# Performance work log

Hardware: AMD Instinct MI355X
Metric: run time of the kernel (lower is better)

## Reference

```python
import jax, jax.numpy as jnp
import numpy as np

B, L, D, K_LIN, T = 32, 512, 1024, 7, 8  # T = 1 identity ('root') + 7 linear experts


def setup_inputs() -> dict:
    key = jax.random.key(0)
    k0, k1, k2 = jax.random.split(key, 3)
    actions = jax.random.normal(k0, (B, L, D), dtype=jnp.float32)
    action_type = jax.random.randint(k1, (B, L), 0, T)
    W = jax.random.normal(k2, (K_LIN, D, D), dtype=jnp.float32) * 0.02  # (K, out, in)
    b = jnp.zeros((K_LIN, D), dtype=jnp.float32)
    return {"actions": actions, "action_type": action_type, "W": W, "b": b}


def reference(actions, action_type, W, b):
    # Project padded actions through ALL experts (matches original ModuleDict loop).
    # proj: (B, L, K_LIN, D) ; W is (K, out, in) so contract over input dim i.
    proj = jnp.einsum('bli,koi->blko', actions, W) + b[None, None, :, :]
    # 'root' expert is nn.Identity -> stacked first (dict insertion order).
    p = jnp.concatenate([actions[:, :, None, :], proj], axis=2)  # (B, L, T, D)
    # One-hot mask built via scatter in the original == one_hot here.
    mask = jax.nn.one_hot(action_type, T, dtype=p.dtype)[..., None]  # (B, L, T, 1)
    embedded = (mask * p).sum(axis=2)  # (B, L, D)
    return embedded
```

## Files before the change

### kernel.cpp

```cpp
#include <hip/hip_runtime.h>


#define NTOK 16384
#define DDIM 1024
#define NEXP 7
#define BM 256
#define BN 256
#define BK 64
#define NKT (DDIM / BK)

#define WI_OFFS   16
#define WI_NTILES 32
#define WI_TABLE  64
#define WI_CTOK   512
#define WS_ABF_B  1048576
#define WS_WBF_B  (WS_ABF_B + NTOK * DDIM * 2)

typedef __attribute__((ext_vector_type(8))) short short8;
typedef __attribute__((ext_vector_type(4))) float f32x4;

__device__ __forceinline__ unsigned short f2bf(float f) {
    unsigned u = __float_as_uint(f);
    u += 0x7fff + ((u >> 16) & 1);
    return (unsigned short)(u >> 16);
}

__device__ __forceinline__ void gload16(const void* g, void* l) {
    __builtin_amdgcn_global_load_lds(
        (const __attribute__((address_space(1))) void*)g,
        (__attribute__((address_space(3))) void*)l, 16, 0, 0);
}

__global__ __launch_bounds__(1024) void routeconv_k(
    const int* __restrict__ type, int* __restrict__ wsi,
    const float* __restrict__ W, unsigned short* __restrict__ Wbf) {
    const int bid = blockIdx.x, tid = threadIdx.x;
    if (bid == 0) {
        __shared__ int h[16][8];
        __shared__ int base2[16][8];
        const int wave = tid >> 6, lane = tid & 63;
        const unsigned long long lt = (1ULL << lane) - 1;

        const int4* tsrc = (const int4*)(type + tid * 16);
        int4 v0 = tsrc[0], v1 = tsrc[1], v2 = tsrc[2], v3 = tsrc[3];
        int kv[16] = { v0.x, v0.y, v0.z, v0.w, v1.x, v1.y, v1.z, v1.w,
                       v2.x, v2.y, v2.z, v2.w, v3.x, v3.y, v3.z, v3.w };

        int cnt[8];
#pragma unroll
        for (int e = 0; e < 8; ++e) cnt[e] = 0;
#pragma unroll
        for (int i = 0; i < 16; ++i) {
#pragma unroll
            for (int e = 0; e < 8; ++e)
                cnt[e] += __popcll(__ballot(kv[i] == e));
        }
        if (lane == 0) {
#pragma unroll
            for (int e = 0; e < 8; ++e) h[wave][e] = cnt[e];
        }
        __syncthreads();

        if (tid == 0) {
            int acc = 0, t = 0;
            for (int e = 0; e < NEXP; ++e) {
                wsi[WI_OFFS + e] = acc;
                int run = acc;
                for (int w = 0; w < 16; ++w) { base2[w][e + 1] = run; run += h[w][e + 1]; }
                int nt = (run - acc + BM - 1) >> 8;
                for (int i = 0; i < nt; ++i) {
                    wsi[WI_TABLE + 2 * t] = e;
                    wsi[WI_TABLE + 2 * t + 1] = acc + i * BM;
                    ++t;
                }
                acc = run;
            }
            wsi[WI_OFFS + NEXP] = acc;
            wsi[WI_NTILES] = t;
            int run = acc;
            for (int w = 0; w < 16; ++w) { base2[w][0] = run; run += h[w][0]; }
        }
        __syncthreads();

        int rb[8];
#pragma unroll
        for (int e = 0; e < 8; ++e) rb[e] = base2[wave][e];
#pragma unroll
        for (int i = 0; i < 16; ++i) {
            int k = kv[i];
            int pos = 0;
#pragma unroll
            for (int e = 0; e < 8; ++e) {
                unsigned long long m = __ballot(k == e);
                int p = rb[e] + __popcll(m & lt);
                pos = (k == e) ? p : pos;
                rb[e] += __popcll(m);
            }
            wsi[WI_CTOK + pos] = tid * 16 + i;
        }
    } else {
        size_t i = ((size_t)(bid - 1) * 1024 + tid) * 16;
        const float4* src = (const float4*)(W + i);
        float4 v0 = src[0], v1 = src[1], v2 = src[2], v3 = src[3];
        short8 h0, h1;
        h0[0]=f2bf(v0.x); h0[1]=f2bf(v0.y); h0[2]=f2bf(v0.z); h0[3]=f2bf(v0.w);
        h0[4]=f2bf(v1.x); h0[5]=f2bf(v1.y); h0[6]=f2bf(v1.z); h0[7]=f2bf(v1.w);
        h1[0]=f2bf(v2.x); h1[1]=f2bf(v2.y); h1[2]=f2bf(v2.z); h1[3]=f2bf(v2.w);
        h1[4]=f2bf(v3.x); h1[5]=f2bf(v3.y); h1[6]=f2bf(v3.z); h1[7]=f2bf(v3.w);
        *(short8*)(Wbf + i) = h0;
        *(short8*)(Wbf + i + 8) = h1;
    }
}

__global__ __launch_bounds__(256) void aconv_k(
    const float* __restrict__ A, const int* __restrict__ wsi,
    unsigned short* __restrict__ Abf, float* __restrict__ out) {
    const int wave = threadIdx.x >> 6, lane = threadIdx.x & 63;
    const int s = blockIdx.x * 4 + wave;
    const int nlin = wsi[WI_OFFS + NEXP];
    const int tok = wsi[WI_CTOK + s];
    const float4* src = (const float4*)(A + (size_t)tok * DDIM);
    if (s >= nlin) {
        float4* d = (float4*)(out + (size_t)tok * DDIM);
#pragma unroll
        for (int j = 0; j < 4; ++j) d[lane + j * 64] = src[lane + j * 64];
    } else {
        float4 v0 = src[lane * 4 + 0], v1 = src[lane * 4 + 1];
        float4 v2 = src[lane * 4 + 2], v3 = src[lane * 4 + 3];
        short8 h0, h1;
        h0[0]=f2bf(v0.x); h0[1]=f2bf(v0.y); h0[2]=f2bf(v0.z); h0[3]=f2bf(v0.w);
        h0[4]=f2bf(v1.x); h0[5]=f2bf(v1.y); h0[6]=f2bf(v1.z); h0[7]=f2bf(v1.w);
        h1[0]=f2bf(v2.x); h1[1]=f2bf(v2.y); h1[2]=f2bf(v2.z); h1[3]=f2bf(v2.w);
        h1[4]=f2bf(v3.x); h1[5]=f2bf(v3.y); h1[6]=f2bf(v3.z); h1[7]=f2bf(v3.w);
        unsigned short* d = Abf + (size_t)s * DDIM + lane * 16;
        *(short8*)d = h0;
        *(short8*)(d + 8) = h1;
    }
}

#define TILE(Abase, Bbase, sNA, sNB, KT)                           \
    do {                                                           \
        short8 a1[8], b1[4];                                       \
        _Pragma("unroll")                                          \
        for (int m = 0; m < 8; ++m)                                \
            a1[m] = *(const short8*)(Abase + sl0 + m * 2048);      \
        _Pragma("unroll")                                          \
        for (int n = 0; n < 4; ++n)                                \
            b1[n] = *(const short8*)(Bbase + sl0 + n * 2048);      \
        if ((KT) + 1 < NKT) {                                      \
            const int ke_ = ((KT) + 1) * BK;                       \
            _Pragma("unroll")                                      \
            for (int q = 0; q < 4; ++q)                            \
                gload16(aSrc[q] + ke_, sNA + q * 8192);            \
            _Pragma("unroll")                                      \
            for (int q = 0; q < 4; ++q)                            \
                gload16(bSrc[q] + ke_, sNB + q * 8192);            \
        }                                                          \
        __builtin_amdgcn_s_setprio(1);                             \
        _Pragma("unroll")                                          \
        for (int m = 0; m < 8; ++m)                                \
            _Pragma("unroll")                                      \
            for (int n = 0; n < 4; ++n)                            \
                acc[m][n] = __builtin_amdgcn_mfma_f32_16x16x32_bf16(\
                    a1[m], b1[n], acc[m][n], 0, 0, 0);             \
        __builtin_amdgcn_s_setprio(0);                             \
        short8 a2[8], b2[4];                                       \
        _Pragma("unroll")                                          \
        for (int m = 0; m < 8; ++m)                                \
            a2[m] = *(const short8*)(Abase + sl1 + m * 2048);      \
        _Pragma("unroll")                                          \
        for (int n = 0; n < 4; ++n)                                \
            b2[n] = *(const short8*)(Bbase + sl1 + n * 2048);      \
        __builtin_amdgcn_s_setprio(1);                             \
        _Pragma("unroll")                                          \
        for (int m = 0; m < 8; ++m)                                \
            _Pragma("unroll")                                      \
            for (int n = 0; n < 4; ++n)                            \
                acc[m][n] = __builtin_amdgcn_mfma_f32_16x16x32_bf16(\
                    a2[m], b2[n], acc[m][n], 0, 0, 0);             \
        __builtin_amdgcn_s_setprio(0);                             \
        asm volatile("s_waitcnt vmcnt(0)" ::: "memory");           \
        __builtin_amdgcn_s_barrier();                              \
    } while (0)

__global__ __launch_bounds__(512, 2) void gemm_k(
    const unsigned short* __restrict__ Abf,
    const unsigned short* __restrict__ Wbf,
    const float* __restrict__ bias, float* __restrict__ out,
    const int* __restrict__ wsi) {
    const int bid = blockIdx.x;
    const int c = bid & 7;
    const int g = bid >> 3;
    const int ntiles = wsi[WI_NTILES];
    const int* offs = wsi + WI_OFFS;
    const int* tab  = wsi + WI_TABLE;
    const int* ctok = wsi + WI_CTOK;

    __shared__ unsigned short As0[BM * BK];
    __shared__ unsigned short As1[BM * BK];
    __shared__ unsigned short Bs0[BM * BK];
    __shared__ unsigned short Bs1[BM * BK];

    const int tid = threadIdx.x, lane = tid & 63, wave = tid >> 6;
    const int wr = wave >> 2, wc = wave & 3;
    const int lane15 = lane & 15;
    const int srow = lane >> 3;
    const int schunk = ((lane & 7) ^ srow) * 8;

    const int sl0 = (((lane >> 4)) ^ (lane & 7)) * 16;
    const int sl1 = ((4 | (lane >> 4)) ^ (lane & 7)) * 16;
    const char* aR0 = (const char*)As0 + wr * 16384 + lane15 * 128;
    const char* aR1 = (const char*)As1 + wr * 16384 + lane15 * 128;
    const char* bR0 = (const char*)Bs0 + wc * 8192 + lane15 * 128;
    const char* bR1 = (const char*)Bs1 + wc * 8192 + lane15 * 128;
    char* sA0 = (char*)As0 + wave * 1024;
    char* sA1 = (char*)As1 + wave * 1024;
    char* sB0 = (char*)Bs0 + wave * 1024;
    char* sB1 = (char*)Bs1 + wave * 1024;

    for (int rep = 0; rep < 2; ++rep) {
        const int q4 = g + 32 * rep;
        const int ty = (q4 >> 2) * 8 + c;
        const int tx = q4 & 3;
        if (ty >= ntiles) break;

        const int e     = tab[2 * ty];
        const int crow0 = tab[2 * ty + 1];
        const int nend  = offs[e + 1];
        const int col0  = tx * BN;
        const unsigned short* Wb = Wbf + (size_t)e * DDIM * DDIM;

        const unsigned short* aSrc[4];
        const unsigned short* bSrc[4];
#pragma unroll
        for (int q = 0; q < 4; ++q) {
            int r = min(crow0 + q * 64 + wave * 8 + srow, NTOK - 1);
            aSrc[q] = Abf + (size_t)r * DDIM + schunk;
            bSrc[q] = Wb + (size_t)(col0 + q * 64 + wave * 8 + srow) * DDIM + schunk;
        }

        f32x4 acc[8][4];
#pragma unroll
        for (int m = 0; m < 8; ++m)
#pragma unroll
            for (int n = 0; n < 4; ++n) acc[m][n] = (f32x4){0.f, 0.f, 0.f, 0.f};

#pragma unroll
        for (int q = 0; q < 4; ++q) gload16(aSrc[q], sA0 + q * 8192);
#pragma unroll
        for (int q = 0; q < 4; ++q) gload16(bSrc[q], sB0 + q * 8192);
        asm volatile("s_waitcnt vmcnt(0)" ::: "memory");
        __builtin_amdgcn_s_barrier();

        for (int kt2 = 0; kt2 < NKT / 2; ++kt2) {
            TILE(aR0, bR0, sA1, sB1, 2 * kt2);
            TILE(aR1, bR1, sA0, sB0, 2 * kt2 + 1);
        }

        const int crow4 = (lane >> 4) * 4;
        float bv[4];
#pragma unroll
        for (int n = 0; n < 4; ++n)
            bv[n] = bias[e * DDIM + col0 + wc * 64 + n * 16 + lane15];

#pragma unroll
        for (int m = 0; m < 8; ++m) {
#pragma unroll
            for (int r = 0; r < 4; ++r) {
                int gr = crow0 + wr * 128 + m * 16 + crow4 + r;
                if (gr >= nend) continue;
                int tok = ctok[gr];
                float* orow = out + (size_t)tok * DDIM + col0 + wc * 64 + lane15;
#pragma unroll
                for (int n = 0; n < 4; ++n)
                    orow[n * 16] = acc[m][n][r] + bv[n];
            }
        }
        __builtin_amdgcn_s_barrier();
    }
}

extern "C" void kernel_launch(void* const* d_in, const int* in_sizes, int n_in,
                              void* d_out, int out_size, void* d_ws, size_t ws_size,
                              hipStream_t stream) {
    const float* actions = (const float*)d_in[0];
    const int*   atype   = (const int*)d_in[1];
    const float* W       = (const float*)d_in[2];
    const float* bias    = (const float*)d_in[3];
    float* out = (float*)d_out;

    int* wsi = (int*)d_ws;
    unsigned short* Abf = (unsigned short*)((char*)d_ws + WS_ABF_B);
    unsigned short* Wbf = (unsigned short*)((char*)d_ws + WS_WBF_B);

    routeconv_k<<<1 + 448, 1024, 0, stream>>>(atype, wsi, W, Wbf);
    aconv_k<<<NTOK / 4, 256, 0, stream>>>(actions, wsi, Abf, out);
    gemm_k<<<256, 512, 0, stream>>>(Abf, Wbf, bias, out, wsi);
}
```

Baseline: 82.42 us.

## Fuse activation conversion into routing kernel and gather rows in GEMM

```diff
diff --git a/kernel.cpp b/kernel.cpp
--- a/kernel.cpp
+++ b/kernel.cpp
@@ -31,9 +31,11 @@
         (__attribute__((address_space(3))) void*)l, 16, 0, 0);
 }
 
-__global__ __launch_bounds__(1024) void routeconv_k(
+__global__ __launch_bounds__(1024) void prep_k(
     const int* __restrict__ type, int* __restrict__ wsi,
-    const float* __restrict__ W, unsigned short* __restrict__ Wbf) {
+    const float* __restrict__ W, unsigned short* __restrict__ Wbf,
+    const float* __restrict__ A, unsigned short* __restrict__ Abf,
+    float* __restrict__ out) {
     const int bid = blockIdx.x, tid = threadIdx.x;
     if (bid == 0) {
         __shared__ int h[16][8];
@@ -52,7 +54,7 @@
 #pragma unroll
         for (int i = 0; i < 16; ++i) {
 #pragma unroll
-            for (int e = 0; e < 8; ++e)
+            for (int e = 1; e < 8; ++e)
                 cnt[e] += __popcll(__ballot(kv[i] == e));
         }
         if (lane == 0) {
@@ -77,28 +79,26 @@
             }
             wsi[WI_OFFS + NEXP] = acc;
             wsi[WI_NTILES] = t;
-            int run = acc;
-            for (int w = 0; w < 16; ++w) { base2[w][0] = run; run += h[w][0]; }
         }
         __syncthreads();
 
         int rb[8];
 #pragma unroll
-        for (int e = 0; e < 8; ++e) rb[e] = base2[wave][e];
+        for (int e = 1; e < 8; ++e) rb[e] = base2[wave][e];
 #pragma unroll
         for (int i = 0; i < 16; ++i) {
             int k = kv[i];
-            int pos = 0;
-#pragma unroll
-            for (int e = 0; e < 8; ++e) {
+            int pos = -1;
+#pragma unroll
+            for (int e = 1; e < 8; ++e) {
                 unsigned long long m = __ballot(k == e);
                 int p = rb[e] + __popcll(m & lt);
                 pos = (k == e) ? p : pos;
                 rb[e] += __popcll(m);
             }
-            wsi[WI_CTOK + pos] = tid * 16 + i;
-        }
-    } else {
+            if (k > 0) wsi[WI_CTOK + pos] = tid * 16 + i;
+        }
+    } else if (bid <= 448) {
         size_t i = ((size_t)(bid - 1) * 1024 + tid) * 16;
         const float4* src = (const float4*)(W + i);
         float4 v0 = src[0], v1 = src[1], v2 = src[2], v3 = src[3];
@@ -109,32 +109,26 @@
         h1[4]=f2bf(v3.x); h1[5]=f2bf(v3.y); h1[6]=f2bf(v3.z); h1[7]=f2bf(v3.w);
         *(short8*)(Wbf + i) = h0;
         *(short8*)(Wbf + i + 8) = h1;
-    }
-}
-
-__global__ __launch_bounds__(256) void aconv_k(
-    const float* __restrict__ A, const int* __restrict__ wsi,
-    unsigned short* __restrict__ Abf, float* __restrict__ out) {
-    const int wave = threadIdx.x >> 6, lane = threadIdx.x & 63;
-    const int s = blockIdx.x * 4 + wave;
-    const int nlin = wsi[WI_OFFS + NEXP];
-    const int tok = wsi[WI_CTOK + s];
-    const float4* src = (const float4*)(A + (size_t)tok * DDIM);
-    if (s >= nlin) {
-        float4* d = (float4*)(out + (size_t)tok * DDIM);
-#pragma unroll
-        for (int j = 0; j < 4; ++j) d[lane + j * 64] = src[lane + j * 64];
     } else {
-        float4 v0 = src[lane * 4 + 0], v1 = src[lane * 4 + 1];
-        float4 v2 = src[lane * 4 + 2], v3 = src[lane * 4 + 3];
-        short8 h0, h1;
-        h0[0]=f2bf(v0.x); h0[1]=f2bf(v0.y); h0[2]=f2bf(v0.z); h0[3]=f2bf(v0.w);
-        h0[4]=f2bf(v1.x); h0[5]=f2bf(v1.y); h0[6]=f2bf(v1.z); h0[7]=f2bf(v1.w);
-        h1[0]=f2bf(v2.x); h1[1]=f2bf(v2.y); h1[2]=f2bf(v2.z); h1[3]=f2bf(v2.w);
-        h1[4]=f2bf(v3.x); h1[5]=f2bf(v3.y); h1[6]=f2bf(v3.z); h1[7]=f2bf(v3.w);
-        unsigned short* d = Abf + (size_t)s * DDIM + lane * 16;
-        *(short8*)d = h0;
-        *(short8*)(d + 8) = h1;
+        const int wave = tid >> 6, lane = tid & 63;
+        const int t = (bid - 449) * 16 + wave;
+        const float4* src = (const float4*)(A + (size_t)t * DDIM);
+        if (type[t] == 0) {
+            float4* d = (float4*)(out + (size_t)t * DDIM);
+#pragma unroll
+            for (int j = 0; j < 4; ++j) d[lane + j * 64] = src[lane + j * 64];
+        } else {
+            float4 v0 = src[lane * 4 + 0], v1 = src[lane * 4 + 1];
+            float4 v2 = src[lane * 4 + 2], v3 = src[lane * 4 + 3];
+            short8 h0, h1;
+            h0[0]=f2bf(v0.x); h0[1]=f2bf(v0.y); h0[2]=f2bf(v0.z); h0[3]=f2bf(v0.w);
+            h0[4]=f2bf(v1.x); h0[5]=f2bf(v1.y); h0[6]=f2bf(v1.z); h0[7]=f2bf(v1.w);
+            h1[0]=f2bf(v2.x); h1[1]=f2bf(v2.y); h1[2]=f2bf(v2.z); h1[3]=f2bf(v2.w);
+            h1[4]=f2bf(v3.x); h1[5]=f2bf(v3.y); h1[6]=f2bf(v3.z); h1[7]=f2bf(v3.w);
+            unsigned short* d = Abf + (size_t)t * DDIM + lane * 16;
+            *(short8*)d = h0;
+            *(short8*)(d + 8) = h1;
+        }
     }
 }
 
@@ -195,6 +189,7 @@
     const int* offs = wsi + WI_OFFS;
     const int* tab  = wsi + WI_TABLE;
     const int* ctok = wsi + WI_CTOK;
+    const int nlin  = offs[NEXP];
 
     __shared__ unsigned short As0[BM * BK];
     __shared__ unsigned short As1[BM * BK];
@@ -234,8 +229,8 @@
         const unsigned short* bSrc[4];
 #pragma unroll
         for (int q = 0; q < 4; ++q) {
-            int r = min(crow0 + q * 64 + wave * 8 + srow, NTOK - 1);
-            aSrc[q] = Abf + (size_t)r * DDIM + schunk;
+            int r = min(crow0 + q * 64 + wave * 8 + srow, nlin - 1);
+            aSrc[q] = Abf + (size_t)ctok[r] * DDIM + schunk;
             bSrc[q] = Wb + (size_t)(col0 + q * 64 + wave * 8 + srow) * DDIM + schunk;
         }
 
@@ -293,7 +288,6 @@
     unsigned short* Abf = (unsigned short*)((char*)d_ws + WS_ABF_B);
     unsigned short* Wbf = (unsigned short*)((char*)d_ws + WS_WBF_B);
 
-    routeconv_k<<<1 + 448, 1024, 0, stream>>>(atype, wsi, W, Wbf);
-    aconv_k<<<NTOK / 4, 256, 0, stream>>>(actions, wsi, Abf, out);
+    prep_k<<<1473, 1024, 0, stream>>>(atype, wsi, W, Wbf, actions, Abf, out);
     gemm_k<<<256, 512, 0, stream>>>(Abf, Wbf, bias, out, wsi);
 }
```

Result: faster. 69.44 us (median of 2 runs) (-15.7%).
